# Kernel tuning notes

Measured on AMD Instinct MI355X. Metric: run time of the kernel, lower is better.

The kernel has to match this reference:

```python
import jax, jax.numpy as jnp
import numpy as np

N, E, D, H, DH, FF, C, L = 50000, 640000, 128, 8, 16, 256, 5, 6
EPS = 1e-5


def _bn(x, g, b):
    # training-mode BatchNorm1d over the node dimension
    m = jnp.mean(x, axis=0)
    v = jnp.var(x, axis=0)
    return (x - m) * jax.lax.rsqrt(v + EPS) * g + b


def _sparse_mha(x, src, dst, Wq, Wk, Wv, Wo):
    # edge-restricted multi-head attention: softmax over incoming edges per dst node
    q = (x @ Wq).reshape(N, H, DH)
    k = (x @ Wk).reshape(N, H, DH)
    v = (x @ Wv).reshape(N, H, DH)
    s = jnp.einsum('ehd,ehd->eh', q[dst], k[src]) * (1.0 / np.sqrt(DH))  # [E,H]
    smax = jax.ops.segment_max(s, dst, num_segments=N)
    smax = jnp.where(jnp.isfinite(smax), smax, 0.0)  # guard isolated nodes
    e = jnp.exp(s - smax[dst])
    den = jax.ops.segment_sum(e, dst, num_segments=N)
    alpha = e / jnp.where(den > 0, den, 1.0)[dst]
    out = jax.ops.segment_sum(alpha[:, :, None] * v[src], dst, num_segments=N)  # [N,H,DH]
    return out.reshape(N, D) @ Wo


def setup_inputs() -> dict:
    key = jax.random.key(0)
    ks = jax.random.split(key, 18)
    f = lambda k, shp, sc: (jax.random.normal(k, shp, jnp.float32) * sc)
    return {
        'x': jax.random.normal(ks[0], (N, D), jnp.float32),
        'edge_index': jax.random.randint(ks[1], (2, E), 0, N),
        'Wq': f(ks[2], (L, D, D), 0.08),
        'Wk': f(ks[3], (L, D, D), 0.08),
        'Wv': f(ks[4], (L, D, D), 0.08),
        'Wo': f(ks[5], (L, D, D), 0.08),
        'g1': jnp.ones((L, D), jnp.float32),
        'bn1': jnp.zeros((L, D), jnp.float32),
        'W1': f(ks[6], (L, D, FF), 0.08),
        'bf1': jnp.zeros((L, FF), jnp.float32),
        'W2': f(ks[7], (L, FF, D), 0.06),
        'bf2': jnp.zeros((L, D), jnp.float32),
        'g2': jnp.ones((L, D), jnp.float32),
        'bn2': jnp.zeros((L, D), jnp.float32),
        'Wp': f(ks[8], (D, C), 0.08),
        'bp': jnp.zeros((C,), jnp.float32),
    }


def reference(x, edge_index, Wq, Wk, Wv, Wo, g1, bn1, W1, bf1, W2, bf2, g2, bn2, Wp, bp):
    src, dst = edge_index[0], edge_index[1]
    for i in range(L):  # fixed small layer count
        res = x  # residual is Identity (num_input == num_output)
        a = _sparse_mha(x, src, dst, Wq[i], Wk[i], Wv[i], Wo[i])
        x = _bn(a + res, g1[i], bn1[i])
        h = jax.nn.relu(x @ W1[i] + bf1[i])  # leakiness=0 -> relu
        x = _bn(x + (h @ W2[i] + bf2[i]), g2[i], bn2[i])
    node_pred = x @ Wp + bp
    return node_pred
```

## Files before the change

### kernel.cpp

```cpp
#include <hip/hip_runtime.h>
#include <hip/hip_bf16.h>
#include <cstdio>

#define NN 50000
#define EE 640000
#define DD 128
#define HH 8
#define DH 16
#define FFD 256
#define CC 5
#define LL 6
#define EPSV 1e-5f

typedef __attribute__((ext_vector_type(8))) short bf16x8;
typedef __attribute__((ext_vector_type(8))) unsigned short ushort8;
typedef __attribute__((ext_vector_type(4))) float f32x4;

__device__ __forceinline__ float bfu2f(unsigned short u) {
  union { unsigned int i; float f; } x; x.i = ((unsigned int)u) << 16; return x.f;
}
__device__ __forceinline__ unsigned short f2bf(float f) {
  union { float f; unsigned int i; } x; x.f = f;
  unsigned int r = (x.i + 0x7fffu + ((x.i >> 16) & 1u)) >> 16;
  return (unsigned short)r;
}

__global__ void detect_kernel(const unsigned int* __restrict__ g1w, int* __restrict__ flag) {
  if (threadIdx.x == 0 && blockIdx.x == 0) *flag = (g1w[0] == 0x3F803F80u) ? 1 : 0;
}

struct ConvJobs { const void* in[8]; float* out[8]; int n[8]; };
__global__ __launch_bounds__(256) void convert_batch_kernel(ConvJobs jobs, const int* __restrict__ flag) {
  int b = blockIdx.x;
  const void* in = jobs.in[b];
  float* out = jobs.out[b];
  int n = jobs.n[b];
  int use_bf = *flag;
  for (int i = threadIdx.x; i < n; i += 256) {
    if (use_bf) out[i] = bfu2f(((const unsigned short*)in)[i]);
    else        out[i] = ((const float*)in)[i];
  }
}

__global__ __launch_bounds__(256) void to_bf16_kernel(const void* __restrict__ in,
                                                      unsigned short* __restrict__ out, int n,
                                                      const int* __restrict__ flag) {
  int i = blockIdx.x * blockDim.x + threadIdx.x;
  if (i >= n) return;
  if (*flag) out[i] = ((const unsigned short*)in)[i];
  else       out[i] = f2bf(((const float*)in)[i]);
}

__global__ __launch_bounds__(256) void t_qkv_tiled(const void* __restrict__ wq, const void* __restrict__ wk,
                                                   const void* __restrict__ wv,
                                                   unsigned short* __restrict__ qkvT,
                                                   const int* __restrict__ flag) {
  __shared__ unsigned short tile[32][33];
  int l = blockIdx.z / 3, which = blockIdx.z % 3;
  const void* in = (which == 0) ? wq : (which == 1) ? wk : wv;
  size_t off = (size_t)l * DD * DD;
  unsigned short* out = qkvT + (size_t)l * 384 * DD + (size_t)which * DD * DD;
  int tx = threadIdx.x & 31, ty = threadIdx.x >> 5;
  int k0 = blockIdx.x * 32, n0 = blockIdx.y * 32;
  int use_bf = *flag;
#pragma unroll
  for (int i = 0; i < 4; i++) {
    int k = k0 + ty + i * 8;
    unsigned short v;
    if (use_bf) v = ((const unsigned short*)in)[off + (size_t)k * DD + n0 + tx];
    else        v = f2bf(((const float*)in)[off + (size_t)k * DD + n0 + tx]);
    tile[ty + i * 8][tx] = v;
  }
  __syncthreads();
#pragma unroll
  for (int i = 0; i < 4; i++) {
    int n = n0 + ty + i * 8;
    out[(size_t)n * DD + k0 + tx] = tile[tx][ty + i * 8];
  }
}

__global__ __launch_bounds__(256) void t_w_tiled(const void* __restrict__ in,
                                                 unsigned short* __restrict__ out,
                                                 int K, int N, const int* __restrict__ flag) {
  __shared__ unsigned short tile[32][33];
  int l = blockIdx.z;
  size_t off = (size_t)l * K * N;
  unsigned short* o = out + (size_t)l * K * N;
  int tx = threadIdx.x & 31, ty = threadIdx.x >> 5;
  int k0 = blockIdx.x * 32, n0 = blockIdx.y * 32;
  int use_bf = *flag;
#pragma unroll
  for (int i = 0; i < 4; i++) {
    int k = k0 + ty + i * 8;
    unsigned short v;
    if (use_bf) v = ((const unsigned short*)in)[off + (size_t)k * N + n0 + tx];
    else        v = f2bf(((const float*)in)[off + (size_t)k * N + n0 + tx]);
    tile[ty + i * 8][tx] = v;
  }
  __syncthreads();
#pragma unroll
  for (int i = 0; i < 4; i++) {
    int n = n0 + ty + i * 8;
    o[(size_t)n * K + k0 + tx] = tile[tx][ty + i * 8];
  }
}

__global__ __launch_bounds__(256) void zero_kernel(int* __restrict__ p, int n) {
  int i = blockIdx.x * blockDim.x + threadIdx.x;
  if (i < n) p[i] = 0;
}

__global__ __launch_bounds__(256) void count_kernel(const int* __restrict__ dst, int* __restrict__ counts) {
  int e = blockIdx.x * blockDim.x + threadIdx.x;
  if (e < EE) atomicAdd(&counts[dst[e]], 1);
}

__global__ __launch_bounds__(256) void scan1_kernel(const int* __restrict__ counts,
                                                    int* __restrict__ row_ptr, int* __restrict__ partials) {
  __shared__ int sh[256];
  int t = threadIdx.x;
  int i = blockIdx.x * 256 + t;
  int v = (i < NN) ? counts[i] : 0;
  sh[t] = v; __syncthreads();
#pragma unroll
  for (int off = 1; off < 256; off <<= 1) {
    int u = (t >= off) ? sh[t - off] : 0;
    __syncthreads();
    sh[t] += u;
    __syncthreads();
  }
  if (i < NN) row_ptr[i] = sh[t] - v;
  if (t == 255) partials[blockIdx.x] = sh[t];
}

__global__ __launch_bounds__(256) void scan2_kernel(int* __restrict__ partials, int nb) {
  __shared__ int sh[256];
  int t = threadIdx.x;
  int v = (t < nb) ? partials[t] : 0;
  sh[t] = v; __syncthreads();
#pragma unroll
  for (int off = 1; off < 256; off <<= 1) {
    int u = (t >= off) ? sh[t - off] : 0;
    __syncthreads();
    sh[t] += u;
    __syncthreads();
  }
  if (t < nb) partials[t] = sh[t] - v;
}

__global__ __launch_bounds__(256) void scan3_kernel(int* __restrict__ row_ptr, const int* __restrict__ partials) {
  int i = blockIdx.x * 256 + threadIdx.x;
  if (i < NN) row_ptr[i] += partials[blockIdx.x];
  if (i == 0) row_ptr[NN] = EE;
}

__global__ __launch_bounds__(256) void fill_kernel(const int* __restrict__ src, const int* __restrict__ dst,
                                                   const int* __restrict__ row_ptr, int* __restrict__ cursor,
                                                   int* __restrict__ csr_src) {
  int e = blockIdx.x * blockDim.x + threadIdx.x;
  if (e < EE) {
    int d = dst[e];
    int pos = row_ptr[d] + atomicAdd(&cursor[d], 1);
    csr_src[pos] = src[e];
  }
}

template<int K, bool RELU, bool HASBIAS, bool HASRES, bool OUTBF, bool STATS>
__global__ __launch_bounds__(256) void mfma_gemm(const unsigned short* __restrict__ A,
                                                 const unsigned short* __restrict__ BT,
                                                 const float* __restrict__ bias,
                                                 const unsigned short* __restrict__ resid,
                                                 void* __restrict__ C, float* __restrict__ stats,
                                                 int M, int ldc) {
  __shared__ float lsum[128];
  __shared__ float lsq[128];
  int tid = threadIdx.x;
  int lane = tid & 63, wave = tid >> 6;
  int m0 = blockIdx.x * 64 + (wave >> 1) * 32;
  int n0 = blockIdx.y * 128 + (wave & 1) * 64;
  int lm = lane & 15;
  int quad = lane >> 4;
  int kq = quad * 8;

  int rowA[2];
#pragma unroll
  for (int r = 0; r < 2; r++) {
    int rr = m0 + 16 * r + lm;
    rowA[r] = (rr < M) ? rr : (M - 1);
  }
  const unsigned short* aptr0 = A + (size_t)rowA[0] * K + kq;
  const unsigned short* aptr1 = A + (size_t)rowA[1] * K + kq;
  const unsigned short* bptr[4];
#pragma unroll
  for (int c = 0; c < 4; c++)
    bptr[c] = BT + (size_t)(n0 + 16 * c + lm) * K + kq;

  f32x4 acc[2][4];
#pragma unroll
  for (int r = 0; r < 2; r++)
#pragma unroll
    for (int c = 0; c < 4; c++) acc[r][c] = (f32x4){0.f, 0.f, 0.f, 0.f};

#pragma unroll
  for (int k0 = 0; k0 < K; k0 += 32) {
    bf16x8 a[2], b[4];
    a[0] = *(const bf16x8*)(aptr0 + k0);
    a[1] = *(const bf16x8*)(aptr1 + k0);
#pragma unroll
    for (int c = 0; c < 4; c++)
      b[c] = *(const bf16x8*)(bptr[c] + k0);
#pragma unroll
    for (int r = 0; r < 2; r++)
#pragma unroll
      for (int c = 0; c < 4; c++)
        acc[r][c] = __builtin_amdgcn_mfma_f32_16x16x32_bf16(b[c], a[r], acc[r][c], 0, 0, 0);
  }

  if (STATS) {
    if (tid < 128) { lsum[tid] = 0.f; lsq[tid] = 0.f; }
    __syncthreads();
  }

  float st_s[4][4], st_q[4][4];
  if (STATS) {
#pragma unroll
    for (int c = 0; c < 4; c++)
#pragma unroll
      for (int reg = 0; reg < 4; reg++) { st_s[c][reg] = 0.f; st_q[c][reg] = 0.f; }
  }

#pragma unroll
  for (int r = 0; r < 2; r++) {
    int row = m0 + 16 * r + lm;
    if (row >= M) continue;
#pragma unroll
    for (int c = 0; c < 4; c++) {
      int col = n0 + 16 * c + quad * 4;
      float4 bv = HASBIAS ? *(const float4*)(bias + col) : make_float4(0.f, 0.f, 0.f, 0.f);
      float o[4];
      o[0] = acc[r][c][0] + bv.x; o[1] = acc[r][c][1] + bv.y;
      o[2] = acc[r][c][2] + bv.z; o[3] = acc[r][c][3] + bv.w;
      if (HASRES) {
        ushort4 rr = *(const ushort4*)(resid + (size_t)row * ldc + col);
        o[0] += bfu2f(rr.x); o[1] += bfu2f(rr.y); o[2] += bfu2f(rr.z); o[3] += bfu2f(rr.w);
      }
      if (RELU) {
        o[0] = fmaxf(o[0], 0.f); o[1] = fmaxf(o[1], 0.f);
        o[2] = fmaxf(o[2], 0.f); o[3] = fmaxf(o[3], 0.f);
      }
      size_t idx = (size_t)row * ldc + col;
      if (OUTBF) {
        ushort4 w;
        w.x = f2bf(o[0]); w.y = f2bf(o[1]); w.z = f2bf(o[2]); w.w = f2bf(o[3]);
        *(ushort4*)((unsigned short*)C + idx) = w;
      } else {
        *(float4*)((float*)C + idx) = make_float4(o[0], o[1], o[2], o[3]);
      }
      if (STATS) {
#pragma unroll
        for (int reg = 0; reg < 4; reg++) {
          st_s[c][reg] += o[reg];
          st_q[c][reg] = fmaf(o[reg], o[reg], st_q[c][reg]);
        }
      }
    }
  }

  if (STATS) {
#pragma unroll
    for (int c = 0; c < 4; c++)
#pragma unroll
      for (int reg = 0; reg < 4; reg++) {
        float s = st_s[c][reg], q = st_q[c][reg];
        s += __shfl_xor(s, 1);  q += __shfl_xor(q, 1);
        s += __shfl_xor(s, 2);  q += __shfl_xor(q, 2);
        s += __shfl_xor(s, 4);  q += __shfl_xor(q, 4);
        s += __shfl_xor(s, 8);  q += __shfl_xor(q, 8);
        if (lm == 0) {
          int cl = (wave & 1) * 64 + 16 * c + quad * 4 + reg;
          atomicAdd(&lsum[cl], s);
          atomicAdd(&lsq[cl], q);
        }
      }
    __syncthreads();
    if (tid < 128) {
      atomicAdd(&stats[tid], lsum[tid]);
      atomicAdd(&stats[128 + tid], lsq[tid]);
    }
  }
}

__global__ __launch_bounds__(256) void attn_kernel(const unsigned short* __restrict__ qkv,
                                                   const int* __restrict__ row_ptr,
                                                   const int* __restrict__ csr_src,
                                                   unsigned short* __restrict__ t1) {
  int t = blockIdx.x * blockDim.x + threadIdx.x;
  int half = t & 1;
  int nh = t >> 1;
  int n = nh >> 3, h = nh & 7;
  const unsigned short* qp = qkv + (size_t)n * 384 + h * 16 + half * 8;
  float qf[8];
  {
    bf16x8 q0 = *(const bf16x8*)qp;
#pragma unroll
    for (int i = 0; i < 8; i++) qf[i] = bfu2f((unsigned short)q0[i]);
  }
  float m = -3.0e38f, l = 0.f;
  float A[8];
#pragma unroll
  for (int i = 0; i < 8; i++) A[i] = 0.f;
  int e0 = row_ptr[n], e1 = row_ptr[n + 1];
  if (e0 < e1) {
    int s = csr_src[e0];
    const unsigned short* kp = qkv + (size_t)s * 384 + 128 + h * 16 + half * 8;
    bf16x8 k0 = *(const bf16x8*)kp;
    bf16x8 v0 = *(const bf16x8*)(kp + 128);
    for (int e = e0; e < e1; e++) {
      int sn = csr_src[(e + 1 < e1) ? e + 1 : e];
      const unsigned short* kpn = qkv + (size_t)sn * 384 + 128 + h * 16 + half * 8;
      bf16x8 nk0 = *(const bf16x8*)kpn;
      bf16x8 nv0 = *(const bf16x8*)(kpn + 128);

      float part = 0.f;
#pragma unroll
      for (int i = 0; i < 8; i++) part += qf[i] * bfu2f((unsigned short)k0[i]);
      float sc = (part + __shfl_xor(part, 1)) * 0.25f;
      float mn = fmaxf(m, sc);
      float cf = __expf(m - mn);
      float p  = __expf(sc - mn);
      l = l * cf + p;
#pragma unroll
      for (int i = 0; i < 8; i++)
        A[i] = A[i] * cf + p * bfu2f((unsigned short)v0[i]);
      m = mn;
      k0 = nk0; v0 = nv0;
    }
  }
  float inv = (l > 0.f) ? 1.f / l : 0.f;
  ushort8 o0;
#pragma unroll
  for (int i = 0; i < 8; i++) o0[i] = f2bf(A[i] * inv);
  unsigned short* op = t1 + (size_t)n * 128 + h * 16 + half * 8;
  *(ushort8*)op = o0;
}

__global__ __launch_bounds__(256) void bn_apply_kernel(const ushort4* __restrict__ y4,
                                                       const float* __restrict__ statsL,
                                                       const float* __restrict__ g,
                                                       const float* __restrict__ b,
                                                       ushort4* __restrict__ xb) {
  __shared__ float ssc[128];
  __shared__ float ssh[128];
  int t = threadIdx.x;
  if (t < 128) {
    float mean = statsL[t] * (1.f / NN);
    float var  = statsL[128 + t] * (1.f / NN) - mean * mean;
    var = fmaxf(var, 0.f);
    float sc = g[t] * rsqrtf(var + EPSV);
    ssc[t] = sc;
    ssh[t] = b[t] - mean * sc;
  }
  __syncthreads();
  int i = blockIdx.x * 256 + t;
  const int total = NN * (DD / 4);
  if (i >= total) return;
  int c4 = (i & 31) * 4;
  ushort4 v = y4[i];
  ushort4 o;
  o.x = f2bf(fmaf(bfu2f(v.x), ssc[c4 + 0], ssh[c4 + 0]));
  o.y = f2bf(fmaf(bfu2f(v.y), ssc[c4 + 1], ssh[c4 + 1]));
  o.z = f2bf(fmaf(bfu2f(v.z), ssc[c4 + 2], ssh[c4 + 2]));
  o.w = f2bf(fmaf(bfu2f(v.w), ssc[c4 + 3], ssh[c4 + 3]));
  xb[i] = o;
}

__global__ __launch_bounds__(256) void proj_kernel(const unsigned short* __restrict__ x,
                                                   const float* __restrict__ Wp,
                                                   const float* __restrict__ bp,
                                                   void* __restrict__ out,
                                                   const int* __restrict__ flag) {
  __shared__ float W[DD * CC];
  __shared__ float bias[CC];
  for (int i = threadIdx.x; i < DD * CC; i += 256) W[i] = Wp[i];
  if (threadIdx.x < CC) bias[threadIdx.x] = bp[threadIdx.x];
  __syncthreads();
  int n = blockIdx.x * blockDim.x + threadIdx.x;
  if (n >= NN) return;
  float acc[CC];
#pragma unroll
  for (int c = 0; c < CC; c++) acc[c] = bias[c];
  const ushort4* xp = (const ushort4*)(x + (size_t)n * DD);
#pragma unroll
  for (int k4 = 0; k4 < DD / 4; k4++) {
    ushort4 u = xp[k4];
    float a0 = bfu2f(u.x), a1 = bfu2f(u.y), a2 = bfu2f(u.z), a3 = bfu2f(u.w);
    const float* w = &W[k4 * 4 * CC];
#pragma unroll
    for (int c = 0; c < CC; c++)
      acc[c] += a0 * w[c] + a1 * w[CC + c] + a2 * w[2 * CC + c] + a3 * w[3 * CC + c];
  }
  if (*flag) {
    __hip_bfloat16* o16 = (__hip_bfloat16*)out;
#pragma unroll
    for (int c = 0; c < CC; c++) o16[(size_t)n * CC + c] = __float2bfloat16(acc[c]);
  } else {
    float* o32 = (float*)out;
#pragma unroll
    for (int c = 0; c < CC; c++) o32[(size_t)n * CC + c] = acc[c];
  }
}

extern "C" void kernel_launch(void* const* d_in, const int* in_sizes, int n_in,
                              void* d_out, int out_size, void* d_ws, size_t ws_size,
                              hipStream_t stream) {
  const int* ei = (const int*)d_in[1];

  char* p = (char*)d_ws;
  auto carve = [&](size_t bytes) { char* r = p; p += (bytes + 255) & ~(size_t)255; return (void*)r; };
  unsigned short* xb   = (unsigned short*)carve((size_t)NN * DD * 2);
  unsigned short* qkv  = (unsigned short*)carve((size_t)NN * 384 * 2);
  unsigned short* t1   = (unsigned short*)carve((size_t)NN * DD * 2);
  unsigned short* hbuf = (unsigned short*)carve((size_t)NN * FFD * 2);
  unsigned short* y    = (unsigned short*)carve((size_t)NN * DD * 2);
  float* stats = (float*)carve(12 * 256 * 4);
  int* row_ptr = (int*)carve((size_t)(NN + 1) * 4);
  int* cursor  = (int*)carve((size_t)NN * 4);
  int* counts  = (int*)carve((size_t)NN * 4);
  int* csr_src = (int*)carve((size_t)EE * 4);
  int* flag    = (int*)carve(256);
  int* partials = (int*)carve(256 * 4);
  unsigned short* qkvT = (unsigned short*)carve((size_t)LL * 384 * DD * 2);
  unsigned short* WoT  = (unsigned short*)carve((size_t)LL * DD * DD * 2);
  unsigned short* W1T  = (unsigned short*)carve((size_t)LL * FFD * DD * 2);
  unsigned short* W2T  = (unsigned short*)carve((size_t)LL * DD * FFD * 2);
  float* g1_f  = (float*)carve((size_t)LL * DD * 4);
  float* bn1_f = (float*)carve((size_t)LL * DD * 4);
  float* bf1_f = (float*)carve((size_t)LL * FFD * 4);
  float* bf2_f = (float*)carve((size_t)LL * DD * 4);
  float* g2_f  = (float*)carve((size_t)LL * DD * 4);
  float* bn2_f = (float*)carve((size_t)LL * DD * 4);
  float* Wp_f  = (float*)carve((size_t)DD * CC * 4);
  float* bp_f  = (float*)carve((size_t)CC * 4);
  size_t need = (size_t)(p - (char*)d_ws);
  if (need > ws_size) {
    fprintf(stderr, "kernel_launch: workspace too small: need %zu, have %zu\n", need, ws_size);
    return;
  }

  const int* src  = ei;
  const int* dstp = ei + EE;

  detect_kernel<<<1, 64, 0, stream>>>((const unsigned int*)d_in[6], flag);
  to_bf16_kernel<<<(NN * DD + 255) / 256, 256, 0, stream>>>(d_in[0], xb, NN * DD, flag);

  {
    ConvJobs j;
    j.in[0] = d_in[6];  j.out[0] = g1_f;  j.n[0] = LL * DD;
    j.in[1] = d_in[7];  j.out[1] = bn1_f; j.n[1] = LL * DD;
    j.in[2] = d_in[9];  j.out[2] = bf1_f; j.n[2] = LL * FFD;
    j.in[3] = d_in[11]; j.out[3] = bf2_f; j.n[3] = LL * DD;
    j.in[4] = d_in[12]; j.out[4] = g2_f;  j.n[4] = LL * DD;
    j.in[5] = d_in[13]; j.out[5] = bn2_f; j.n[5] = LL * DD;
    j.in[6] = d_in[14]; j.out[6] = Wp_f;  j.n[6] = DD * CC;
    j.in[7] = d_in[15]; j.out[7] = bp_f;  j.n[7] = CC;
    convert_batch_kernel<<<8, 256, 0, stream>>>(j, flag);
  }

  t_qkv_tiled<<<dim3(4, 4, 3 * LL), 256, 0, stream>>>(d_in[2], d_in[3], d_in[4], qkvT, flag);
  t_w_tiled<<<dim3(4, 4, LL), 256, 0, stream>>>(d_in[5], WoT, DD, DD, flag);
  t_w_tiled<<<dim3(4, 8, LL), 256, 0, stream>>>(d_in[8], W1T, DD, FFD, flag);
  t_w_tiled<<<dim3(8, 4, LL), 256, 0, stream>>>(d_in[10], W2T, FFD, DD, flag);

  zero_kernel<<<12, 256, 0, stream>>>((int*)stats, 12 * 256);
  zero_kernel<<<(NN + 255) / 256, 256, 0, stream>>>(counts, NN);
  zero_kernel<<<(NN + 255) / 256, 256, 0, stream>>>(cursor, NN);

  const int NB = (NN + 255) / 256;
  count_kernel<<<(EE + 255) / 256, 256, 0, stream>>>(dstp, counts);
  scan1_kernel<<<NB, 256, 0, stream>>>(counts, row_ptr, partials);
  scan2_kernel<<<1, 256, 0, stream>>>(partials, NB);
  scan3_kernel<<<NB, 256, 0, stream>>>(row_ptr, partials);
  fill_kernel<<<(EE + 255) / 256, 256, 0, stream>>>(src, dstp, row_ptr, cursor, csr_src);

  const int gm = (NN + 63) / 64;
  for (int layer = 0; layer < LL; layer++) {
    const unsigned short* qkvT_l = qkvT + (size_t)layer * 384 * DD;
    const unsigned short* WoT_l  = WoT  + (size_t)layer * DD * DD;
    const unsigned short* W1T_l  = W1T  + (size_t)layer * FFD * DD;
    const unsigned short* W2T_l  = W2T  + (size_t)layer * DD * FFD;
    float* st1 = stats + (size_t)(layer * 2 + 0) * 256;
    float* st2 = stats + (size_t)(layer * 2 + 1) * 256;

    mfma_gemm<128, false, false, false, true, false><<<dim3(gm, 3), 256, 0, stream>>>(
        xb, qkvT_l, nullptr, nullptr, qkv, nullptr, NN, 384);
    attn_kernel<<<NN * HH * 2 / 256, 256, 0, stream>>>(qkv, row_ptr, csr_src, t1);
    mfma_gemm<128, false, false, true, true, true><<<dim3(gm, 1), 256, 0, stream>>>(
        t1, WoT_l, nullptr, xb, y, st1, NN, 128);
    bn_apply_kernel<<<(NN * 32 + 255) / 256, 256, 0, stream>>>(
        (const ushort4*)y, st1, g1_f + (size_t)layer * DD, bn1_f + (size_t)layer * DD, (ushort4*)xb);

    mfma_gemm<128, true, true, false, true, false><<<dim3(gm, 2), 256, 0, stream>>>(
        xb, W1T_l, bf1_f + (size_t)layer * FFD, nullptr, hbuf, nullptr, NN, 256);
    mfma_gemm<256, false, true, true, true, true><<<dim3(gm, 1), 256, 0, stream>>>(
        hbuf, W2T_l, bf2_f + (size_t)layer * DD, xb, y, st2, NN, 128);
    bn_apply_kernel<<<(NN * 32 + 255) / 256, 256, 0, stream>>>(
        (const ushort4*)y, st2, g2_f + (size_t)layer * DD, bn2_f + (size_t)layer * DD, (ushort4*)xb);
  }

  proj_kernel<<<(NN + 255) / 256, 256, 0, stream>>>(xb, Wp_f, bp_f, d_out, flag);
}
```

Before: 1.485 ms.

## Fold BatchNorm affine into next GEMM weights and drop bn_apply passes

Removes the two per-layer bn_apply passes by folding each BatchNorm scale and shift into the next GEMM's weights and bias with a small fold_kernel. The residual add applies the pending affine in the epilogue, and the last BN is applied inside proj_kernel. The GEMM tile changes to 128 rows by 64 columns with a 4-step K chunk for more loads in flight, and attention prefetches two edges ahead. Rounding the scaled weights to bf16 adds some numerical error, and each layer now launches extra small serial fold kernels.

```diff
diff --git a/kernel.cpp b/kernel.cpp
--- a/kernel.cpp
+++ b/kernel.cpp
@@ -110,6 +110,16 @@
   if (i < n) p[i] = 0;
 }
 
+__global__ void init_id_kernel(float* __restrict__ stats_id, float* __restrict__ g_id, float* __restrict__ b_id) {
+  int t = threadIdx.x;
+  if (t < 128) {
+    stats_id[t] = 0.f;
+    stats_id[128 + t] = (float)NN * (1.0f - EPSV);
+    g_id[t] = 1.f;
+    b_id[t] = 0.f;
+  }
+}
+
 __global__ __launch_bounds__(256) void count_kernel(const int* __restrict__ dst, int* __restrict__ counts) {
   int e = blockIdx.x * blockDim.x + threadIdx.x;
   if (e < EE) atomicAdd(&counts[dst[e]], 1);
@@ -165,19 +175,51 @@
   }
 }
 
-template<int K, bool RELU, bool HASBIAS, bool HASRES, bool OUTBF, bool STATS>
+__global__ __launch_bounds__(128) void fold_kernel(const float* __restrict__ stats,
+                                                   const float* __restrict__ g,
+                                                   const float* __restrict__ b,
+                                                   const unsigned short* __restrict__ WT,
+                                                   const float* __restrict__ base_bias,
+                                                   unsigned short* __restrict__ WTo,
+                                                   float* __restrict__ bias_o,
+                                                   float* __restrict__ ss_o) {
+  __shared__ float ssc[128];
+  __shared__ float ssh[128];
+  __shared__ float part[2];
+  int t = threadIdx.x;
+  float mean = stats[t] * (1.f / NN);
+  float var  = fmaxf(stats[128 + t] * (1.f / NN) - mean * mean, 0.f);
+  float sc = g[t] * rsqrtf(var + EPSV);
+  float sh = b[t] - mean * sc;
+  ssc[t] = sc; ssh[t] = sh;
+  if (blockIdx.x == 0) { ss_o[t] = sc; ss_o[128 + t] = sh; }
+  __syncthreads();
+  int c = blockIdx.x;
+  float w = bfu2f(WT[(size_t)c * 128 + t]);
+  WTo[(size_t)c * 128 + t] = f2bf(ssc[t] * w);
+  float contrib = ssh[t] * w;
+#pragma unroll
+  for (int off = 32; off; off >>= 1) contrib += __shfl_down(contrib, off);
+  if ((t & 63) == 0) part[t >> 6] = contrib;
+  __syncthreads();
+  if (t == 0) bias_o[c] = (base_bias ? base_bias[c] : 0.f) + part[0] + part[1];
+}
+
+template<int K, bool RELU, bool HASBIAS, bool RESAFF, bool STATS>
 __global__ __launch_bounds__(256) void mfma_gemm(const unsigned short* __restrict__ A,
                                                  const unsigned short* __restrict__ BT,
                                                  const float* __restrict__ bias,
                                                  const unsigned short* __restrict__ resid,
-                                                 void* __restrict__ C, float* __restrict__ stats,
+                                                 const float* __restrict__ rss,
+                                                 unsigned short* __restrict__ C,
+                                                 float* __restrict__ stats,
                                                  int M, int ldc) {
-  __shared__ float lsum[128];
-  __shared__ float lsq[128];
+  __shared__ float lsum[64];
+  __shared__ float lsq[64];
   int tid = threadIdx.x;
   int lane = tid & 63, wave = tid >> 6;
-  int m0 = blockIdx.x * 64 + (wave >> 1) * 32;
-  int n0 = blockIdx.y * 128 + (wave & 1) * 64;
+  int m0 = blockIdx.x * 128 + wave * 32;
+  int n0 = blockIdx.y * 64;
   int lm = lane & 15;
   int quad = lane >> 4;
   int kq = quad * 8;
@@ -202,22 +244,29 @@
     for (int c = 0; c < 4; c++) acc[r][c] = (f32x4){0.f, 0.f, 0.f, 0.f};
 
 #pragma unroll
-  for (int k0 = 0; k0 < K; k0 += 32) {
-    bf16x8 a[2], b[4];
-    a[0] = *(const bf16x8*)(aptr0 + k0);
-    a[1] = *(const bf16x8*)(aptr1 + k0);
+  for (int kc = 0; kc < K; kc += 128) {
+    bf16x8 a[2][4], b[4][4];
+#pragma unroll
+    for (int ks = 0; ks < 4; ks++) {
+      a[0][ks] = *(const bf16x8*)(aptr0 + kc + ks * 32);
+      a[1][ks] = *(const bf16x8*)(aptr1 + kc + ks * 32);
+    }
 #pragma unroll
     for (int c = 0; c < 4; c++)
-      b[c] = *(const bf16x8*)(bptr[c] + k0);
-#pragma unroll
-    for (int r = 0; r < 2; r++)
-#pragma unroll
-      for (int c = 0; c < 4; c++)
-        acc[r][c] = __builtin_amdgcn_mfma_f32_16x16x32_bf16(b[c], a[r], acc[r][c], 0, 0, 0);
+#pragma unroll
+      for (int ks = 0; ks < 4; ks++)
+        b[c][ks] = *(const bf16x8*)(bptr[c] + kc + ks * 32);
+#pragma unroll
+    for (int ks = 0; ks < 4; ks++)
+#pragma unroll
+      for (int r = 0; r < 2; r++)
+#pragma unroll
+        for (int c = 0; c < 4; c++)
+          acc[r][c] = __builtin_amdgcn_mfma_f32_16x16x32_bf16(b[c][ks], a[r][ks], acc[r][c], 0, 0, 0);
   }
 
   if (STATS) {
-    if (tid < 128) { lsum[tid] = 0.f; lsq[tid] = 0.f; }
+    if (tid < 64) { lsum[tid] = 0.f; lsq[tid] = 0.f; }
     __syncthreads();
   }
 
@@ -240,22 +289,23 @@
       float o[4];
       o[0] = acc[r][c][0] + bv.x; o[1] = acc[r][c][1] + bv.y;
       o[2] = acc[r][c][2] + bv.z; o[3] = acc[r][c][3] + bv.w;
-      if (HASRES) {
+      if (RESAFF) {
         ushort4 rr = *(const ushort4*)(resid + (size_t)row * ldc + col);
-        o[0] += bfu2f(rr.x); o[1] += bfu2f(rr.y); o[2] += bfu2f(rr.z); o[3] += bfu2f(rr.w);
+        float4 rsc = *(const float4*)(rss + col);
+        float4 rsh = *(const float4*)(rss + 128 + col);
+        o[0] += bfu2f(rr.x) * rsc.x + rsh.x;
+        o[1] += bfu2f(rr.y) * rsc.y + rsh.y;
+        o[2] += bfu2f(rr.z) * rsc.z + rsh.z;
+        o[3] += bfu2f(rr.w) * rsc.w + rsh.w;
       }
       if (RELU) {
         o[0] = fmaxf(o[0], 0.f); o[1] = fmaxf(o[1], 0.f);
         o[2] = fmaxf(o[2], 0.f); o[3] = fmaxf(o[3], 0.f);
       }
       size_t idx = (size_t)row * ldc + col;
-      if (OUTBF) {
-        ushort4 w;
-        w.x = f2bf(o[0]); w.y = f2bf(o[1]); w.z = f2bf(o[2]); w.w = f2bf(o[3]);
-        *(ushort4*)((unsigned short*)C + idx) = w;
-      } else {
-        *(float4*)((float*)C + idx) = make_float4(o[0], o[1], o[2], o[3]);
-      }
+      ushort4 w;
+      w.x = f2bf(o[0]); w.y = f2bf(o[1]); w.z = f2bf(o[2]); w.w = f2bf(o[3]);
+      *(ushort4*)(C + idx) = w;
       if (STATS) {
 #pragma unroll
         for (int reg = 0; reg < 4; reg++) {
@@ -277,15 +327,14 @@
         s += __shfl_xor(s, 4);  q += __shfl_xor(q, 4);
         s += __shfl_xor(s, 8);  q += __shfl_xor(q, 8);
         if (lm == 0) {
-          int cl = (wave & 1) * 64 + 16 * c + quad * 4 + reg;
-          atomicAdd(&lsum[cl], s);
-          atomicAdd(&lsq[cl], q);
+          atomicAdd(&lsum[16 * c + quad * 4 + reg], s);
+          atomicAdd(&lsq[16 * c + quad * 4 + reg], q);
         }
       }
     __syncthreads();
-    if (tid < 128) {
-      atomicAdd(&stats[tid], lsum[tid]);
-      atomicAdd(&stats[128 + tid], lsq[tid]);
+    if (tid < 64) {
+      atomicAdd(&stats[n0 + tid], lsum[tid]);
+      atomicAdd(&stats[128 + n0 + tid], lsq[tid]);
     }
   }
 }
@@ -311,19 +360,27 @@
   for (int i = 0; i < 8; i++) A[i] = 0.f;
   int e0 = row_ptr[n], e1 = row_ptr[n + 1];
   if (e0 < e1) {
-    int s = csr_src[e0];
-    const unsigned short* kp = qkv + (size_t)s * 384 + 128 + h * 16 + half * 8;
-    bf16x8 k0 = *(const bf16x8*)kp;
-    bf16x8 v0 = *(const bf16x8*)(kp + 128);
+    int last = e1 - 1;
+    const size_t hoff = 128 + h * 16 + half * 8;
+    int s0 = csr_src[e0];
+    const unsigned short* kp0 = qkv + (size_t)s0 * 384 + hoff;
+    bf16x8 ck = *(const bf16x8*)kp0;
+    bf16x8 cv = *(const bf16x8*)(kp0 + 128);
+    int ei1 = (e0 + 1 <= last) ? e0 + 1 : last;
+    int s1 = csr_src[ei1];
+    const unsigned short* kp1 = qkv + (size_t)s1 * 384 + hoff;
+    bf16x8 nk = *(const bf16x8*)kp1;
+    bf16x8 nv = *(const bf16x8*)(kp1 + 128);
     for (int e = e0; e < e1; e++) {
-      int sn = csr_src[(e + 1 < e1) ? e + 1 : e];
-      const unsigned short* kpn = qkv + (size_t)sn * 384 + 128 + h * 16 + half * 8;
-      bf16x8 nk0 = *(const bf16x8*)kpn;
-      bf16x8 nv0 = *(const bf16x8*)(kpn + 128);
+      int e2 = (e + 2 <= last) ? e + 2 : last;
+      int s2 = csr_src[e2];
+      const unsigned short* kp2 = qkv + (size_t)s2 * 384 + hoff;
+      bf16x8 k2 = *(const bf16x8*)kp2;
+      bf16x8 v2 = *(const bf16x8*)(kp2 + 128);
 
       float part = 0.f;
 #pragma unroll
-      for (int i = 0; i < 8; i++) part += qf[i] * bfu2f((unsigned short)k0[i]);
+      for (int i = 0; i < 8; i++) part += qf[i] * bfu2f((unsigned short)ck[i]);
       float sc = (part + __shfl_xor(part, 1)) * 0.25f;
       float mn = fmaxf(m, sc);
       float cf = __expf(m - mn);
@@ -331,9 +388,9 @@
       l = l * cf + p;
 #pragma unroll
       for (int i = 0; i < 8; i++)
-        A[i] = A[i] * cf + p * bfu2f((unsigned short)v0[i]);
+        A[i] = A[i] * cf + p * bfu2f((unsigned short)cv[i]);
       m = mn;
-      k0 = nk0; v0 = nv0;
+      ck = nk; cv = nv; nk = k2; nv = v2;
     }
   }
   float inv = (l > 0.f) ? 1.f / l : 0.f;
@@ -344,57 +401,44 @@
   *(ushort8*)op = o0;
 }
 
-__global__ __launch_bounds__(256) void bn_apply_kernel(const ushort4* __restrict__ y4,
-                                                       const float* __restrict__ statsL,
-                                                       const float* __restrict__ g,
-                                                       const float* __restrict__ b,
-                                                       ushort4* __restrict__ xb) {
-  __shared__ float ssc[128];
-  __shared__ float ssh[128];
-  int t = threadIdx.x;
-  if (t < 128) {
-    float mean = statsL[t] * (1.f / NN);
-    float var  = statsL[128 + t] * (1.f / NN) - mean * mean;
-    var = fmaxf(var, 0.f);
-    float sc = g[t] * rsqrtf(var + EPSV);
-    ssc[t] = sc;
-    ssh[t] = b[t] - mean * sc;
-  }
-  __syncthreads();
-  int i = blockIdx.x * 256 + t;
-  const int total = NN * (DD / 4);
-  if (i >= total) return;
-  int c4 = (i & 31) * 4;
-  ushort4 v = y4[i];
-  ushort4 o;
-  o.x = f2bf(fmaf(bfu2f(v.x), ssc[c4 + 0], ssh[c4 + 0]));
-  o.y = f2bf(fmaf(bfu2f(v.y), ssc[c4 + 1], ssh[c4 + 1]));
-  o.z = f2bf(fmaf(bfu2f(v.z), ssc[c4 + 2], ssh[c4 + 2]));
-  o.w = f2bf(fmaf(bfu2f(v.w), ssc[c4 + 3], ssh[c4 + 3]));
-  xb[i] = o;
-}
-
-__global__ __launch_bounds__(256) void proj_kernel(const unsigned short* __restrict__ x,
+__global__ __launch_bounds__(256) void proj_kernel(const unsigned short* __restrict__ y2,
+                                                   const float* __restrict__ statsL,
+                                                   const float* __restrict__ g,
+                                                   const float* __restrict__ b,
                                                    const float* __restrict__ Wp,
                                                    const float* __restrict__ bp,
                                                    void* __restrict__ out,
                                                    const int* __restrict__ flag) {
   __shared__ float W[DD * CC];
   __shared__ float bias[CC];
-  for (int i = threadIdx.x; i < DD * CC; i += 256) W[i] = Wp[i];
-  if (threadIdx.x < CC) bias[threadIdx.x] = bp[threadIdx.x];
+  __shared__ float ssc[128];
+  __shared__ float ssh[128];
+  int t = threadIdx.x;
+  for (int i = t; i < DD * CC; i += 256) W[i] = Wp[i];
+  if (t < CC) bias[t] = bp[t];
+  if (t < 128) {
+    float mean = statsL[t] * (1.f / NN);
+    float var  = fmaxf(statsL[128 + t] * (1.f / NN) - mean * mean, 0.f);
+    float sc = g[t] * rsqrtf(var + EPSV);
+    ssc[t] = sc;
+    ssh[t] = b[t] - mean * sc;
+  }
   __syncthreads();
-  int n = blockIdx.x * blockDim.x + threadIdx.x;
+  int n = blockIdx.x * 256 + t;
   if (n >= NN) return;
   float acc[CC];
 #pragma unroll
   for (int c = 0; c < CC; c++) acc[c] = bias[c];
-  const ushort4* xp = (const ushort4*)(x + (size_t)n * DD);
+  const ushort4* xp = (const ushort4*)(y2 + (size_t)n * DD);
 #pragma unroll
   for (int k4 = 0; k4 < DD / 4; k4++) {
     ushort4 u = xp[k4];
-    float a0 = bfu2f(u.x), a1 = bfu2f(u.y), a2 = bfu2f(u.z), a3 = bfu2f(u.w);
-    const float* w = &W[k4 * 4 * CC];
+    int k = k4 * 4;
+    float a0 = bfu2f(u.x) * ssc[k + 0] + ssh[k + 0];
+    float a1 = bfu2f(u.y) * ssc[k + 1] + ssh[k + 1];
+    float a2 = bfu2f(u.z) * ssc[k + 2] + ssh[k + 2];
+    float a3 = bfu2f(u.w) * ssc[k + 3] + ssh[k + 3];
+    const float* w = &W[k * CC];
 #pragma unroll
     for (int c = 0; c < CC; c++)
       acc[c] += a0 * w[c] + a1 * w[CC + c] + a2 * w[2 * CC + c] + a3 * w[3 * CC + c];
@@ -421,8 +465,14 @@
   unsigned short* qkv  = (unsigned short*)carve((size_t)NN * 384 * 2);
   unsigned short* t1   = (unsigned short*)carve((size_t)NN * DD * 2);
   unsigned short* hbuf = (unsigned short*)carve((size_t)NN * FFD * 2);
-  unsigned short* y    = (unsigned short*)carve((size_t)NN * DD * 2);
-  float* stats = (float*)carve(12 * 256 * 4);
+  unsigned short* y1   = (unsigned short*)carve((size_t)NN * DD * 2);
+  unsigned short* y2   = (unsigned short*)carve((size_t)NN * DD * 2);
+  float* stats  = (float*)carve(12 * 256 * 4);
+  float* stats_id = (float*)carve(256 * 4);
+  float* ss     = (float*)carve(12 * 256 * 4);
+  float* ss_id  = (float*)carve(256 * 4);
+  float* g_id   = (float*)carve(128 * 4);
+  float* b_id   = (float*)carve(128 * 4);
   int* row_ptr = (int*)carve((size_t)(NN + 1) * 4);
   int* cursor  = (int*)carve((size_t)NN * 4);
   int* counts  = (int*)carve((size_t)NN * 4);
@@ -433,6 +483,10 @@
   unsigned short* WoT  = (unsigned short*)carve((size_t)LL * DD * DD * 2);
   unsigned short* W1T  = (unsigned short*)carve((size_t)LL * FFD * DD * 2);
   unsigned short* W2T  = (unsigned short*)carve((size_t)LL * DD * FFD * 2);
+  unsigned short* qkvTf = (unsigned short*)carve((size_t)384 * DD * 2);
+  unsigned short* W1Tf  = (unsigned short*)carve((size_t)FFD * DD * 2);
+  float* qkv_bias = (float*)carve(384 * 4);
+  float* w1_bias  = (float*)carve(256 * 4);
   float* g1_f  = (float*)carve((size_t)LL * DD * 4);
   float* bn1_f = (float*)carve((size_t)LL * DD * 4);
   float* bf1_f = (float*)carve((size_t)LL * FFD * 4);
@@ -472,6 +526,7 @@
   t_w_tiled<<<dim3(8, 4, LL), 256, 0, stream>>>(d_in[10], W2T, FFD, DD, flag);
 
   zero_kernel<<<12, 256, 0, stream>>>((int*)stats, 12 * 256);
+  init_id_kernel<<<1, 128, 0, stream>>>(stats_id, g_id, b_id);
   zero_kernel<<<(NN + 255) / 256, 256, 0, stream>>>(counts, NN);
   zero_kernel<<<(NN + 255) / 256, 256, 0, stream>>>(cursor, NN);
 
@@ -482,30 +537,39 @@
   scan3_kernel<<<NB, 256, 0, stream>>>(row_ptr, partials);
   fill_kernel<<<(EE + 255) / 256, 256, 0, stream>>>(src, dstp, row_ptr, cursor, csr_src);
 
-  const int gm = (NN + 63) / 64;
+  const int gm = (NN + 127) / 128;
   for (int layer = 0; layer < LL; layer++) {
-    const unsigned short* qkvT_l = qkvT + (size_t)layer * 384 * DD;
-    const unsigned short* WoT_l  = WoT  + (size_t)layer * DD * DD;
-    const unsigned short* W1T_l  = W1T  + (size_t)layer * FFD * DD;
-    const unsigned short* W2T_l  = W2T  + (size_t)layer * DD * FFD;
+    const unsigned short* WoT_l = WoT + (size_t)layer * DD * DD;
+    const unsigned short* W1T_l = W1T + (size_t)layer * FFD * DD;
+    const unsigned short* W2T_l = W2T + (size_t)layer * DD * FFD;
     float* st1 = stats + (size_t)(layer * 2 + 0) * 256;
     float* st2 = stats + (size_t)(layer * 2 + 1) * 256;
-
-    mfma_gemm<128, false, false, false, true, false><<<dim3(gm, 3), 256, 0, stream>>>(
-        xb, qkvT_l, nullptr, nullptr, qkv, nullptr, NN, 384);
+    float* ss1 = ss + (size_t)(layer * 2 + 0) * 256;
+
+    const unsigned short* Ain = layer ? y2 : xb;
+    const float* stats_prev = layer ? (stats + (size_t)((layer - 1) * 2 + 1) * 256) : stats_id;
+    const float* g_prev = layer ? (g2_f + (size_t)(layer - 1) * DD) : g_id;
+    const float* b_prev = layer ? (bn2_f + (size_t)(layer - 1) * DD) : b_id;
+    float* ss_prev = layer ? (ss + (size_t)((layer - 1) * 2 + 1) * 256) : ss_id;
+
+    fold_kernel<<<384, 128, 0, stream>>>(stats_prev, g_prev, b_prev,
+                                         qkvT + (size_t)layer * 384 * DD, nullptr,
+                                         qkvTf, qkv_bias, ss_prev);
+    mfma_gemm<128, false, true, false, false><<<dim3(gm, 6), 256, 0, stream>>>(
+        Ain, qkvTf, qkv_bias, nullptr, nullptr, qkv, nullptr, NN, 384);
     attn_kernel<<<NN * HH * 2 / 256, 256, 0, stream>>>(qkv, row_ptr, csr_src, t1);
-    mfma_gemm<128, false, false, true, true, true><<<dim3(gm, 1), 256, 0, stream>>>(
-        t1, WoT_l, nullptr, xb, y, st1, NN, 128);
-    bn_apply_kernel<<<(NN * 32 + 255) / 256, 256, 0, stream>>>(
-        (const ushort4*)y, st1, g1_f + (size_t)layer * DD, bn1_f + (size_t)layer * DD, (ushort4*)xb);
-
-    mfma_gemm<128, true, true, false, true, false><<<dim3(gm, 2), 256, 0, stream>>>(
-        xb, W1T_l, bf1_f + (size_t)layer * FFD, nullptr, hbuf, nullptr, NN, 256);
-    mfma_gemm<256, false, true, true, true, true><<<dim3(gm, 1), 256, 0, stream>>>(
-        hbuf, W2T_l, bf2_f + (size_t)layer * DD, xb, y, st2, NN, 128);
-    bn_apply_kernel<<<(NN * 32 + 255) / 256, 256, 0, stream>>>(
-        (const ushort4*)y, st2, g2_f + (size_t)layer * DD, bn2_f + (size_t)layer * DD, (ushort4*)xb);
-  }
-
-  proj_kernel<<<(NN + 255) / 256, 256, 0, stream>>>(xb, Wp_f, bp_f, d_out, flag);
-}
+    mfma_gemm<128, false, false, true, true><<<dim3(gm, 2), 256, 0, stream>>>(
+        t1, WoT_l, nullptr, Ain, ss_prev, y1, st1, NN, 128);
+    fold_kernel<<<256, 128, 0, stream>>>(st1, g1_f + (size_t)layer * DD, bn1_f + (size_t)layer * DD,
+                                         W1T_l, bf1_f + (size_t)layer * FFD,
+                                         W1Tf, w1_bias, ss1);
+    mfma_gemm<128, true, true, false, false><<<dim3(gm, 4), 256, 0, stream>>>(
+        y1, W1Tf, w1_bias, nullptr, nullptr, hbuf, nullptr, NN, 256);
+    mfma_gemm<256, false, true, true, true><<<dim3(gm, 2), 256, 0, stream>>>(
+        hbuf, W2T_l, bf2_f + (size_t)layer * DD, y1, ss1, y2, st2, NN, 128);
+  }
+
+  proj_kernel<<<(NN + 255) / 256, 256, 0, stream>>>(
+      y2, stats + (size_t)((LL - 1) * 2 + 1) * 256, g2_f + (size_t)(LL - 1) * DD,
+      bn2_f + (size_t)(LL - 1) * DD, Wp_f, bp_f, d_out, flag);
+}
```

New measurement: 1.374 ms. 1.08x faster.
